# Kernel tuning notes

Measured on AMD Instinct MI355X. Metric: run time of the kernel, lower is better.

Reference implementation:

```python
import jax, jax.numpy as jnp
import numpy as np

P_DROP = 0.6  # dropout prob from the source module
N_NODES = 50000
N_EDGES = 800000


def _cheb_edge_weights(edge_index, num_nodes):
    # ChebConv with sym normalization and default lambda_max=2.0:
    # scaled Laplacian hat(L) = 2L/lambda_max - I = -D^{-1/2} A D^{-1/2}
    # (diagonal becomes 0), so edge weight = -1/sqrt(deg[row]*deg[col]).
    row, col = edge_index[0], edge_index[1]
    deg = jnp.zeros((num_nodes,), jnp.float32).at[row].add(1.0)
    dis = jnp.where(deg > 0, jax.lax.rsqrt(jnp.maximum(deg, 1.0)), 0.0)
    return -dis[row] * dis[col]


def _prop(x, row, col, w, n):
    # hat(L) @ x via gather-scale-scatter over the edge list
    return jnp.zeros((n, x.shape[1]), x.dtype).at[row].add(w[:, None] * x[col])


def _cheb_conv(x, row, col, w, W, b, n):
    # Chebyshev recursion: Tx0 = x, Tx1 = hat(L) x, Tx_k = 2 hat(L) Tx_{k-1} - Tx_{k-2}
    Tx0 = x
    out = Tx0 @ W[0]
    Tx1 = _prop(Tx0, row, col, w, n)
    out = out + Tx1 @ W[1]
    for k in range(2, W.shape[0]):
        Tx2 = 2.0 * _prop(Tx1, row, col, w, n) - Tx0
        out = out + Tx2 @ W[k]
        Tx0, Tx1 = Tx1, Tx2
    return out + b


def _dropout(x, key, p):
    keep = jax.random.bernoulli(key, 1.0 - p, x.shape)
    return jnp.where(keep, x * (1.0 / (1.0 - p)), 0.0)


def setup_inputs() -> dict:
    key = jax.random.key(0)
    ks = jax.random.split(key, 8)
    x = jax.random.normal(ks[0], (N_NODES, 64), jnp.float32)
    edge_index = jax.random.randint(ks[1], (2, N_EDGES), 0, N_NODES, jnp.int64)
    W0 = jax.random.normal(ks[2], (2, 64, 64), jnp.float32) * 0.1
    b0 = jnp.zeros((64,), jnp.float32)
    W1 = jax.random.normal(ks[3], (2, 64, 64), jnp.float32) * 0.1
    b1 = jnp.zeros((64,), jnp.float32)
    W2 = jax.random.normal(ks[4], (2, 64, 32), jnp.float32) * 0.1
    b2 = jnp.zeros((32,), jnp.float32)
    return {"x": x, "edge_index": edge_index, "W0": W0, "b0": b0,
            "W1": W1, "b1": b1, "W2": W2, "b2": b2}


def reference(x, edge_index, W0, b0, W1, b1, W2, b2):
    row, col = edge_index[0], edge_index[1]
    n = x.shape[0]
    w = _cheb_edge_weights(edge_index, n)
    dkey = jax.random.key(1)
    params = [(W0, b0), (W1, b1), (W2, b2)]
    for i, (W, b) in enumerate(params):
        x = _dropout(x, jax.random.fold_in(dkey, i), P_DROP)
        x = _cheb_conv(x, row, col, w, W, b, n)
        if i < len(params) - 1:
            x = jax.nn.relu(x)
    return x
```

## Files before the change

### kernel.cpp

```cpp
#include <hip/hip_runtime.h>
#include <stdint.h>

typedef _Float16 half8 __attribute__((ext_vector_type(8)));
typedef float float4v __attribute__((ext_vector_type(4)));

__host__ __device__ inline void tf2x32(uint32_t k0, uint32_t k1,
                                       uint32_t x0, uint32_t x1,
                                       uint32_t* o0, uint32_t* o1) {
  const uint32_t ks2 = k0 ^ k1 ^ 0x1BD11BDAu;
#define ROTL(v, s) (((v) << (s)) | ((v) >> (32 - (s))))
#define RND(r) do { x0 += x1; x1 = ROTL(x1, r); x1 ^= x0; } while (0)
  x0 += k0; x1 += k1;
  RND(13); RND(15); RND(26); RND(6);
  x0 += k1; x1 += ks2 + 1u;
  RND(17); RND(29); RND(16); RND(24);
  x0 += ks2; x1 += k0 + 2u;
  RND(13); RND(15); RND(26); RND(6);
  x0 += k0; x1 += k1 + 3u;
  RND(17); RND(29); RND(16); RND(24);
  x0 += k1; x1 += ks2 + 4u;
  RND(13); RND(15); RND(26); RND(6);
  x0 += ks2; x1 += k0 + 5u;
  *o0 = x0; *o1 = x1;
#undef RND
#undef ROTL
}

__device__ inline bool drop_keep(uint32_t k0, uint32_t k1, uint32_t idx) {
  uint32_t o0, o1;
  tf2x32(k0, k1, 0u, idx, &o0, &o1);
  uint32_t bits = o0 ^ o1;
  float u = __uint_as_float((bits >> 9) | 0x3f800000u) - 1.0f;
  return u < 0.4f;
}

__global__ void k_fill2(const int* __restrict__ row, const int* __restrict__ col,
                        int* __restrict__ cnt, uint16_t* __restrict__ cs,
                        int e, int rows_per_xcd) {
  const int owner = blockIdx.x & 7;
  const int i = (blockIdx.x >> 3) * 256 + threadIdx.x;
  if (i < e) {
    int r = row[i];
    if (r / rows_per_xcd == owner) {
      int pos = atomicAdd(&cnt[r], 1);
      if (pos < 64) cs[(r << 6) + pos] = (uint16_t)col[i];
    }
  }
}

__global__ void k_drop(const float* __restrict__ x, const int* __restrict__ cnt,
                       uint16_t* __restrict__ cs, float* __restrict__ dis,
                       _Float16* __restrict__ y, _Float16* __restrict__ ys,
                       _Float16* __restrict__ ysb, uint32_t k0, uint32_t k1,
                       int n, int nd,
                       const float* __restrict__ W0, const float* __restrict__ W1,
                       const float* __restrict__ W2, _Float16* __restrict__ wh) {
  int i = blockIdx.x * 256 + threadIdx.x;
  if (i < 20480) {
    int d = i;
    if (d < 8192) {
      int o = d >> 7, k = d & 127;
      wh[d] = (_Float16)W0[k * 64 + o];
    } else if (d < 16384) {
      int d1 = d - 8192, o = d1 >> 7, k = d1 & 127;
      wh[d] = (_Float16)W1[k * 64 + o];
    } else {
      int d2 = d - 16384, o = d2 >> 7, k = d2 & 127;
      wh[d] = (_Float16)W2[k * 32 + o];
    }
  }
  if (i < 64) {
    ys[((size_t)n << 6) + i]  = (_Float16)0.f;
    ysb[((size_t)n << 6) + i] = (_Float16)0.f;
  }
  if (i < nd) {
    const int r = i >> 6;
    const int t = i & 63;
    const int d = cnt[r];
    const float dis_r = (d > 0) ? rsqrtf((float)d) : 0.0f;
    float v = drop_keep(k0, k1, (uint32_t)i) ? x[i] * 2.5f : 0.0f;
    y[i]  = (_Float16)v;
    ys[i] = (_Float16)(dis_r * v);
    if (t == 0) dis[r] = dis_r;
    const int cn = d < 64 ? d : 64;
    const int rnd = (cn + 7) & ~7;
    if (t >= cn && t < rnd) cs[(r << 6) + t] = (uint16_t)n;
  }
}

template<int T>
__device__ __forceinline__ void gatherT(int idx_all, int rnd, int g, int sub,
                                        const _Float16* __restrict__ ysg,
                                        uint32_t dummy, float acc[8]) {
  half8 hv[T];
  #pragma unroll
  for (int j = 0; j < T; ++j) {
    int sh = __shfl(idx_all, j * 8 + g, 64);
    uint32_t c = (j * 8 < rnd) ? (uint32_t)(sh & 0xffff) : dummy;
    hv[j] = *(const half8*)((const char*)ysg + (c << 7) + (sub << 4));
  }
  #pragma unroll
  for (int j = 0; j < T; ++j)
    #pragma unroll
    for (int k = 0; k < 8; ++k) acc[k] += (float)hv[j][k];
}

template<int COUT, bool RELU, bool DROPN, bool WBF>
__global__ __launch_bounds__(256, 6) void k_conv(
    const _Float16* __restrict__ yg, const _Float16* __restrict__ ysg,
    const int* __restrict__ cnt, const uint16_t* __restrict__ cs,
    const float* __restrict__ dis, const _Float16* __restrict__ wt,
    const float* __restrict__ b, float* __restrict__ outf,
    _Float16* __restrict__ outb, _Float16* __restrict__ outs,
    uint32_t nk0, uint32_t nk1, int n) {
  constexpr int R  = 16;
  constexpr int TS = 136;
  __shared__ __align__(16) _Float16 xp[R][TS];
  __shared__ float red[4][8][72];

  const int wave = threadIdx.x >> 6;
  const int t    = threadIdx.x & 63;
  const int row0 = blockIdx.x * R;
  const int g    = t >> 3;
  const int sub  = t & 7;
  const uint32_t dummy = (uint32_t)n;

  for (int i = 0; i < 4; ++i) {
    const int rl = wave * 4 + i;
    const int r  = row0 + rl;
    if (r < n) {
      const int d    = cnt[r];
      const int cn   = d < 64 ? d : 64;
      const int rnd  = (cn + 7) & ~7;
      const int base = r << 6;
      const int idx_all = cs[base + t];
      float acc[8] = {0.f, 0.f, 0.f, 0.f, 0.f, 0.f, 0.f, 0.f};
      if (rnd <= 16)      gatherT<2>(idx_all, rnd, g, sub, ysg, dummy, acc);
      else if (rnd <= 32) gatherT<4>(idx_all, rnd, g, sub, ysg, dummy, acc);
      else                gatherT<8>(idx_all, rnd, g, sub, ysg, dummy, acc);
      #pragma unroll
      for (int k = 0; k < 8; ++k) red[wave][k][t] = acc[k];
      __builtin_amdgcn_wave_barrier();
      float s = 0.f;
      #pragma unroll
      for (int g2 = 0; g2 < 8; ++g2) s += red[wave][sub][8 * g2 + g];
      __builtin_amdgcn_wave_barrier();
      xp[rl][t]      = yg[(uint32_t)(r << 6) + t];
      xp[rl][64 + t] = (_Float16)(-dis[r] * s);
    }
  }
  __syncthreads();

  constexpr int NW = COUT / 16;
  const int nn   = t & 15;
  const int quad = t >> 4;
  if (wave < NW) {
    const int colg = wave * 16 + nn;
    float4v acc = {0.f, 0.f, 0.f, 0.f};
    #pragma unroll
    for (int ks = 0; ks < 4; ++ks) {
      half8 a  = *(const half8*)&xp[nn][quad * 8 + 32 * ks];
      half8 bb = *(const half8*)&wt[(size_t)colg * 128 + quad * 8 + 32 * ks];
      acc = __builtin_amdgcn_mfma_f32_16x16x32_f16(a, bb, acc, 0, 0, 0);
    }
    const float bias = b[colg];
    #pragma unroll
    for (int rg = 0; rg < 4; ++rg) {
      const int rl = quad * 4 + rg;
      const int rr = row0 + rl;
      if (rr < n) {
        float v = acc[rg] + bias;
        if (RELU) v = fmaxf(v, 0.0f);
        if (DROPN) {
          if (drop_keep(nk0, nk1, (uint32_t)(rr * 64 + colg))) v *= 2.5f;
          else v = 0.0f;
        }
        if (WBF) {
          outb[(size_t)rr * COUT + colg] = (_Float16)v;
          outs[(size_t)rr * COUT + colg] = (_Float16)(dis[rr] * v);
        } else {
          outf[(size_t)rr * COUT + colg] = v;
        }
      }
    }
  }
}

extern "C" void kernel_launch(void* const* d_in, const int* in_sizes, int n_in,
                              void* d_out, int out_size, void* d_ws, size_t ws_size,
                              hipStream_t stream) {
  const float* x   = (const float*)d_in[0];
  const int*   ei  = (const int*)d_in[1];
  const float* W0  = (const float*)d_in[2];
  const float* b0  = (const float*)d_in[3];
  const float* W1f = (const float*)d_in[4];
  const float* b1  = (const float*)d_in[5];
  const float* W2  = (const float*)d_in[6];
  const float* b2  = (const float*)d_in[7];
  float* out = (float*)d_out;

  const int n = in_sizes[0] / 64;
  const int e = in_sizes[1] / 2;
  const int* row = ei;
  const int* col = ei + e;

  size_t off = 0;
  auto carve = [&](size_t elems) {
    size_t o = off;
    off += (elems + 255) & ~(size_t)255;
    return o;
  };
  int* base = (int*)d_ws;
  int*      cnt = base + carve(n);
  float*    dis = (float*)(base + carve(n));
  uint16_t* cs  = (uint16_t*)(base + carve((size_t)n * 32));
  _Float16* ya  = (_Float16*)(base + carve((size_t)n * 32));
  _Float16* ysa = (_Float16*)(base + carve((size_t)(n + 1) * 32));
  _Float16* yb  = (_Float16*)(base + carve((size_t)n * 32));
  _Float16* ysb = (_Float16*)(base + carve((size_t)(n + 1) * 32));
  _Float16* wh  = (_Float16*)(base + carve(10240));
  (void)ws_size;
  _Float16* wh0 = wh;
  _Float16* wh1 = wh + 8192;
  _Float16* wh2 = wh + 16384;

  uint32_t dk[3][2];
  for (uint32_t i = 0; i < 3; ++i) tf2x32(0u, 1u, 0u, i, &dk[i][0], &dk[i][1]);

  hipMemsetAsync(cnt, 0, (size_t)n * 4, stream);

  const int nchunk = (e + 255) / 256;
  const int bd = ((n * 64) + 255) / 256;
  const int bc = (n + 15) / 16;
  const int rpx = (n + 7) / 8;

  k_fill2<<<nchunk * 8, 256, 0, stream>>>(row, col, cnt, cs, e, rpx);
  k_drop<<<bd, 256, 0, stream>>>(x, cnt, cs, dis, ya, ysa, ysb,
                                 dk[0][0], dk[0][1], n, n * 64,
                                 W0, W1f, W2, wh);

  k_conv<64, true,  true,  true ><<<bc, 256, 0, stream>>>(
      ya, ysa, cnt, cs, dis, wh0, b0, nullptr, yb, ysb, dk[1][0], dk[1][1], n);
  k_conv<64, true,  true,  true ><<<bc, 256, 0, stream>>>(
      yb, ysb, cnt, cs, dis, wh1, b1, nullptr, ya, ysa, dk[2][0], dk[2][1], n);
  k_conv<32, false, false, false><<<bc, 256, 0, stream>>>(
      ya, ysa, cnt, cs, dis, wh2, b2, out, nullptr, nullptr, 0u, 0u, n);
}
```

Before: 193.5 us.

## Prefetch per-row metadata up front and reduce gather partials with cross-lane shuffles

All four rows' column indices, degree counts, norms and self features are now loaded before any gathering starts, so their latencies overlap instead of serialising per row. The LDS scratch array and wave barriers used to reduce the eight partial sums per lane are replaced by a butterfly of shuffle-xor steps that halve the vector at each stage. This cuts LDS traffic and the LDS footprint, which may allow higher occupancy. The cost is more registers held live across the loop, and out-of-range rows are clamped to the last row and recomputed redundantly.

Result: faster. 188.7 us (-2.5%).

```diff
diff --git a/kernel.cpp b/kernel.cpp
--- a/kernel.cpp
+++ b/kernel.cpp
@@ -116,7 +116,6 @@
   constexpr int R  = 16;
   constexpr int TS = 136;
   __shared__ __align__(16) _Float16 xp[R][TS];
-  __shared__ float red[4][8][72];
 
   const int wave = threadIdx.x >> 6;
   const int t    = threadIdx.x & 63;
@@ -125,29 +124,50 @@
   const int sub  = t & 7;
   const uint32_t dummy = (uint32_t)n;
 
+  int      idxs[4], ds4[4];
+  float    dv4[4];
+  _Float16 ygv[4];
+  #pragma unroll
   for (int i = 0; i < 4; ++i) {
+    int r = row0 + wave * 4 + i;
+    r = r < n ? r : n - 1;
+    idxs[i] = cs[(r << 6) + t];
+    ds4[i]  = cnt[r];
+    dv4[i]  = dis[r];
+    ygv[i]  = yg[(uint32_t)(r << 6) + t];
+  }
+
+  #pragma unroll
+  for (int i = 0; i < 4; ++i) {
+    const int cn  = ds4[i] < 64 ? ds4[i] : 64;
+    const int rnd = (cn + 7) & ~7;
+    float acc[8] = {0.f, 0.f, 0.f, 0.f, 0.f, 0.f, 0.f, 0.f};
+    if (rnd <= 16)      gatherT<2>(idxs[i], rnd, g, sub, ysg, dummy, acc);
+    else if (rnd <= 32) gatherT<4>(idxs[i], rnd, g, sub, ysg, dummy, acc);
+    else                gatherT<8>(idxs[i], rnd, g, sub, ysg, dummy, acc);
+
+    const bool b0 = (g & 1), b1 = (g & 2), b2 = (g & 4);
+    float a4[4], a2[2], v;
+    #pragma unroll
+    for (int m = 0; m < 4; ++m) {
+      float keep = b0 ? acc[2 * m + 1] : acc[2 * m];
+      float send = b0 ? acc[2 * m]     : acc[2 * m + 1];
+      a4[m] = keep + __shfl_xor(send, 8, 64);
+    }
+    #pragma unroll
+    for (int m = 0; m < 2; ++m) {
+      float keep = b1 ? a4[2 * m + 1] : a4[2 * m];
+      float send = b1 ? a4[2 * m]     : a4[2 * m + 1];
+      a2[m] = keep + __shfl_xor(send, 16, 64);
+    }
+    {
+      float keep = b2 ? a2[1] : a2[0];
+      float send = b2 ? a2[0] : a2[1];
+      v = keep + __shfl_xor(send, 32, 64);
+    }
     const int rl = wave * 4 + i;
-    const int r  = row0 + rl;
-    if (r < n) {
-      const int d    = cnt[r];
-      const int cn   = d < 64 ? d : 64;
-      const int rnd  = (cn + 7) & ~7;
-      const int base = r << 6;
-      const int idx_all = cs[base + t];
-      float acc[8] = {0.f, 0.f, 0.f, 0.f, 0.f, 0.f, 0.f, 0.f};
-      if (rnd <= 16)      gatherT<2>(idx_all, rnd, g, sub, ysg, dummy, acc);
-      else if (rnd <= 32) gatherT<4>(idx_all, rnd, g, sub, ysg, dummy, acc);
-      else                gatherT<8>(idx_all, rnd, g, sub, ysg, dummy, acc);
-      #pragma unroll
-      for (int k = 0; k < 8; ++k) red[wave][k][t] = acc[k];
-      __builtin_amdgcn_wave_barrier();
-      float s = 0.f;
-      #pragma unroll
-      for (int g2 = 0; g2 < 8; ++g2) s += red[wave][sub][8 * g2 + g];
-      __builtin_amdgcn_wave_barrier();
-      xp[rl][t]      = yg[(uint32_t)(r << 6) + t];
-      xp[rl][64 + t] = (_Float16)(-dis[r] * s);
-    }
+    xp[rl][t]                    = ygv[i];
+    xp[rl][64 + (sub * 8 + g)]   = (_Float16)(-dv4[i] * v);
   }
   __syncthreads();
 
```
